# Kernel optimization log

Hardware: AMD Instinct MI355X
Metric: run time of the kernel (lower is better)

## Reference

```python
import jax, jax.numpy as jnp
import numpy as np

B, C, R, E = 8192, 32, 24, 128
NUM_LOC = 100000
NUM_INNER = 200000   # inner_node_embed has NUM_INNER+1 rows; row 0 is padding_idx
NUM_SLICES = 24


def setup_inputs() -> dict:
    key = jax.random.key(0)
    ks = jax.random.split(key, 7)
    context = jax.random.randint(ks[0], (B, C), 0, NUM_LOC)
    route = jax.random.randint(ks[1], (B, R), 0, NUM_INNER + 1)
    lr = jax.random.randint(ks[2], (B, R), 0, 2)
    slice_idx = jax.random.randint(ks[3], (B,), 0, NUM_SLICES)
    input_embed = jax.random.normal(ks[4], (NUM_LOC, E), dtype=jnp.float32)
    inner_node_embed = jax.random.normal(ks[5], (NUM_INNER + 1, E), dtype=jnp.float32).at[0].set(0.0)
    slice_node_embed = jax.random.uniform(ks[6], (NUM_SLICES, E), dtype=jnp.float32)
    return {
        "context": context, "route": route, "lr": lr, "slice_idx": slice_idx,
        "input_embed": input_embed, "inner_node_embed": inner_node_embed,
        "slice_node_embed": slice_node_embed,
    }


def reference(context, route, lr, slice_idx, input_embed, inner_node_embed, slice_node_embed):
    # context embedding: gather + sum over context window -> (B, E)
    ctx = input_embed[context].sum(axis=1)
    # slice prediction: (B, num_slices) softmax, gather target slice prob -> (B,)
    slice_logits = jnp.einsum('se,be->bs', slice_node_embed, ctx)
    slice_prob = jax.nn.softmax(slice_logits, axis=1)
    slice_pre = jnp.take_along_axis(slice_prob, slice_idx[:, None], axis=1)[:, 0]
    # route scores: (B, R)
    dot = jnp.einsum('bre,be->br', inner_node_embed[route], ctx)
    lr_pre = jax.nn.sigmoid(dot)
    # (2p)^lr - p  -> p if lr==1, (1-p) if lr==0
    route_hidden = jnp.power(2.0 * lr_pre, lr.astype(lr_pre.dtype)) - lr_pre
    # padded route positions (route id == 0) contribute factor 1
    route_hidden = jnp.where(route == 0, jnp.ones((), lr_pre.dtype), route_hidden)
    # per-level product loop collapsed into a single prod over route dim
    pr_route = slice_pre * jnp.prod(route_hidden, axis=1)
    return 1.0 - pr_route.mean()
```

## Files before the change

### kernel.cpp

```cpp
#include <hip/hip_runtime.h>

#define BATCH    8192
#define CTX      32
#define ROUTES   24
#define EDIM     128
#define NSLICE   24
#define WPB      4
#define NBLOCKS  (BATCH / WPB)

__device__ __forceinline__ float packed_sum24(const float (&p)[24], const int lane)
{
    float c[12];
    #pragma unroll
    for (int i = 0; i < 12; ++i) {
        const float e0 = p[2*i]   + __shfl_xor(p[2*i],   32);
        const float e1 = p[2*i+1] + __shfl_xor(p[2*i+1], 32);
        c[i] = (lane & 32) ? e1 : e0;
    }
    float d[6];
    #pragma unroll
    for (int i = 0; i < 6; ++i) {
        const float e0 = c[2*i]   + __shfl_xor(c[2*i],   16);
        const float e1 = c[2*i+1] + __shfl_xor(c[2*i+1], 16);
        d[i] = (lane & 16) ? e1 : e0;
    }
    float e[3];
    #pragma unroll
    for (int i = 0; i < 3; ++i) {
        const float e0 = d[2*i]   + __shfl_xor(d[2*i],   8);
        const float e1 = d[2*i+1] + __shfl_xor(d[2*i+1], 8);
        e[i] = (lane & 8) ? e1 : e0;
    }
    const float f0a = e[0] + __shfl_xor(e[0], 4);
    const float f0b = e[1] + __shfl_xor(e[1], 4);
    const float f0  = (lane & 4) ? f0b : f0a;
    const float f1  = (lane & 4) ? 0.f : (e[2] + __shfl_xor(e[2], 4));
    const float g0 = f0 + __shfl_xor(f0, 2);
    const float g1 = f1 + __shfl_xor(f1, 2);
    float g = (lane & 2) ? g1 : g0;
    g += __shfl_xor(g, 1);
    return g;
}

__global__ __launch_bounds__(256, 4) void tale_fused(
    const int* __restrict__ context,
    const int* __restrict__ route,
    const int* __restrict__ lr,
    const int* __restrict__ slice_idx,
    const float* __restrict__ input_embed,
    const float* __restrict__ inner_node_embed,
    const float* __restrict__ slice_node_embed,
    float* __restrict__ out)
{
    const int tid  = threadIdx.x;
    const int lane = tid & 63;
    const int w    = tid >> 6;
    const int b    = __builtin_amdgcn_readfirstlane(blockIdx.x * WPB + w);

    __shared__ float bs[WPB];

    const int voff = lane << 1;

    const int v = ((lane >> 5) & 1) | (((lane >> 4) & 1) << 1) |
                  (((lane >> 3) & 1) << 2) | (((lane >> 2) & 1) << 3) |
                  (((lane >> 1) & 1) << 4);
    const bool vvalid = (v < ROUTES);
    const int  vcl    = vvalid ? v : 0;

    const int rv = route[b * ROUTES + vcl];
    const int lv = lr[b * ROUTES + vcl];
    const int si = slice_idx[b];

    float a0x=0.f,a0y=0.f,a1x=0.f,a1y=0.f,a2x=0.f,a2y=0.f,a3x=0.f,a3y=0.f;
    #pragma unroll
    for (int i = 0; i < CTX; i += 4) {
        const int i0 = context[b * CTX + i + 0];
        const int i1 = context[b * CTX + i + 1];
        const int i2 = context[b * CTX + i + 2];
        const int i3 = context[b * CTX + i + 3];
        const float2 r0 = *reinterpret_cast<const float2*>(input_embed + (size_t)i0 * EDIM + voff);
        const float2 r1 = *reinterpret_cast<const float2*>(input_embed + (size_t)i1 * EDIM + voff);
        const float2 r2 = *reinterpret_cast<const float2*>(input_embed + (size_t)i2 * EDIM + voff);
        const float2 r3 = *reinterpret_cast<const float2*>(input_embed + (size_t)i3 * EDIM + voff);
        a0x += r0.x; a0y += r0.y;
        a1x += r1.x; a1y += r1.y;
        a2x += r2.x; a2y += r2.y;
        a3x += r3.x; a3y += r3.y;
    }
    const float ax = (a0x + a1x) + (a2x + a3x);
    const float ay = (a0y + a1y) + (a2y + a3y);

    float p[24];
    #pragma unroll
    for (int r = 0; r < ROUTES; ++r) {
        const int idx = route[b * ROUTES + r];
        const float2 t = *reinterpret_cast<const float2*>(
            inner_node_embed + (size_t)idx * EDIM + voff);
        p[r] = t.x * ax + t.y * ay;
    }
    const float dotv = packed_sum24(p, lane);

    float q[24];
    #pragma unroll
    for (int s = 0; s < NSLICE; ++s) {
        const float2 t = *reinterpret_cast<const float2*>(
            slice_node_embed + s * EDIM + voff);
        q[s] = t.x * ax + t.y * ay;
    }
    const float logv = packed_sum24(q, lane);

    const float sg = 1.f / (1.f + __expf(-dotv));
    float h = lv ? sg : (1.f - sg);
    if (!vvalid || rv == 0 || (lane & 1)) h = 1.f;
    h *= __shfl_xor(h, 32);
    h *= __shfl_xor(h, 16);
    h *= __shfl_xor(h, 8);
    h *= __shfl_xor(h, 4);
    h *= __shfl_xor(h, 2);
    h *= __shfl_xor(h, 1);
    const float prodv = h;

    float ml = vvalid ? logv : -3.0e38f;
    ml = fmaxf(ml, __shfl_xor(ml, 32));
    ml = fmaxf(ml, __shfl_xor(ml, 16));
    ml = fmaxf(ml, __shfl_xor(ml, 8));
    ml = fmaxf(ml, __shfl_xor(ml, 4));
    ml = fmaxf(ml, __shfl_xor(ml, 2));
    ml = fmaxf(ml, __shfl_xor(ml, 1));
    float ev = (vvalid && !(lane & 1)) ? __expf(logv - ml) : 0.f;
    float den = ev;
    den += __shfl_xor(den, 32);
    den += __shfl_xor(den, 16);
    den += __shfl_xor(den, 8);
    den += __shfl_xor(den, 4);
    den += __shfl_xor(den, 2);
    den += __shfl_xor(den, 1);
    const int lsel = (((si >> 4) & 1) << 1) | (((si >> 3) & 1) << 2) |
                     (((si >> 2) & 1) << 3) | (((si >> 1) & 1) << 4) |
                     ((si & 1) << 5);
    const float esel = __shfl(ev, lsel);
    const float pr = (esel / den) * prodv;

    if (lane == 0) bs[w] = pr;
    __syncthreads();
    if (tid == 0) {
        const float s = (bs[0] + bs[1]) + (bs[2] + bs[3]);
        atomicAdd(out, 1.0f / NBLOCKS - s * (1.0f / BATCH));
    }
}

extern "C" void kernel_launch(void* const* d_in, const int* in_sizes, int n_in,
                              void* d_out, int out_size, void* d_ws, size_t ws_size,
                              hipStream_t stream)
{
    const int*   context          = (const int*)  d_in[0];
    const int*   route            = (const int*)  d_in[1];
    const int*   lr               = (const int*)  d_in[2];
    const int*   slice_idx        = (const int*)  d_in[3];
    const float* input_embed      = (const float*)d_in[4];
    const float* inner_node_embed = (const float*)d_in[5];
    const float* slice_node_embed = (const float*)d_in[6];
    float* out = (float*)d_out;

    hipMemsetAsync(out, 0, sizeof(float), stream);

    tale_fused<<<NBLOCKS, 64 * WPB, 0, stream>>>(
        context, route, lr, slice_idx,
        input_embed, inner_node_embed, slice_node_embed, out);
}
```

Before: 202.8 us.

## Split wavefront into half-waves with float4 row loads and halved shuffle reductions

Each wavefront now works as two 32-lane halves. Each lane loads a float4 slice of an embedding row, and the two halves handle alternating context, route and slice rows, which replaces the float2 loads where every lane touched every row. This halves the per-lane gather instruction count and roughly halves the shuffle-based packed reduction (12 values per lane instead of 24). It adds a cross-half reduction of the context sum, and launch bounds are raised to 8 blocks per CU to increase occupancy, which could pressure registers.

```diff
diff --git a/kernel.cpp b/kernel.cpp
--- a/kernel.cpp
+++ b/kernel.cpp
@@ -8,41 +8,39 @@
 #define WPB      4
 #define NBLOCKS  (BATCH / WPB)
 
-__device__ __forceinline__ float packed_sum24(const float (&p)[24], const int lane)
+__device__ __forceinline__ float dot4(const float4 a, const float4 b)
 {
-    float c[12];
-    #pragma unroll
-    for (int i = 0; i < 12; ++i) {
-        const float e0 = p[2*i]   + __shfl_xor(p[2*i],   32);
-        const float e1 = p[2*i+1] + __shfl_xor(p[2*i+1], 32);
-        c[i] = (lane & 32) ? e1 : e0;
-    }
-    float d[6];
+    return a.x * b.x + a.y * b.y + a.z * b.z + a.w * b.w;
+}
+
+__device__ __forceinline__ float packed_sum12(const float (&p)[12], const int sub)
+{
+    float c[6];
     #pragma unroll
     for (int i = 0; i < 6; ++i) {
-        const float e0 = c[2*i]   + __shfl_xor(c[2*i],   16);
-        const float e1 = c[2*i+1] + __shfl_xor(c[2*i+1], 16);
-        d[i] = (lane & 16) ? e1 : e0;
+        const float e0 = p[2*i]   + __shfl_xor(p[2*i],   16);
+        const float e1 = p[2*i+1] + __shfl_xor(p[2*i+1], 16);
+        c[i] = (sub & 16) ? e1 : e0;
     }
-    float e[3];
+    float d[3];
     #pragma unroll
     for (int i = 0; i < 3; ++i) {
-        const float e0 = d[2*i]   + __shfl_xor(d[2*i],   8);
-        const float e1 = d[2*i+1] + __shfl_xor(d[2*i+1], 8);
-        e[i] = (lane & 8) ? e1 : e0;
+        const float e0 = c[2*i]   + __shfl_xor(c[2*i],   8);
+        const float e1 = c[2*i+1] + __shfl_xor(c[2*i+1], 8);
+        d[i] = (sub & 8) ? e1 : e0;
     }
-    const float f0a = e[0] + __shfl_xor(e[0], 4);
-    const float f0b = e[1] + __shfl_xor(e[1], 4);
-    const float f0  = (lane & 4) ? f0b : f0a;
-    const float f1  = (lane & 4) ? 0.f : (e[2] + __shfl_xor(e[2], 4));
-    const float g0 = f0 + __shfl_xor(f0, 2);
-    const float g1 = f1 + __shfl_xor(f1, 2);
-    float g = (lane & 2) ? g1 : g0;
+    const float e0a = d[0] + __shfl_xor(d[0], 4);
+    const float e0b = d[1] + __shfl_xor(d[1], 4);
+    const float e0  = (sub & 4) ? e0b : e0a;
+    const float e1  = (sub & 4) ? 0.f : (d[2] + __shfl_xor(d[2], 4));
+    const float f0  = e0 + __shfl_xor(e0, 2);
+    const float f1  = e1 + __shfl_xor(e1, 2);
+    float g = (sub & 2) ? f1 : f0;
     g += __shfl_xor(g, 1);
     return g;
 }
 
-__global__ __launch_bounds__(256, 4) void tale_fused(
+__global__ __launch_bounds__(256, 8) void tale_fused(
     const int* __restrict__ context,
     const int* __restrict__ route,
     const int* __restrict__ lr,
@@ -54,90 +52,97 @@
 {
     const int tid  = threadIdx.x;
     const int lane = tid & 63;
+    const int half = lane >> 5;
+    const int sub  = lane & 31;
     const int w    = tid >> 6;
     const int b    = __builtin_amdgcn_readfirstlane(blockIdx.x * WPB + w);
 
     __shared__ float bs[WPB];
 
-    const int voff = lane << 1;
+    const int v = ((sub >> 4) & 1) | (((sub >> 3) & 1) << 1) |
+                  (((sub >> 2) & 1) << 2) | (((sub >> 1) & 1) << 3);
+    const bool vvalid = (v < 12);
+    const int  d      = 2 * v + half;
+    const int  dcl    = vvalid ? d : 0;
 
-    const int v = ((lane >> 5) & 1) | (((lane >> 4) & 1) << 1) |
-                  (((lane >> 3) & 1) << 2) | (((lane >> 2) & 1) << 3) |
-                  (((lane >> 1) & 1) << 4);
-    const bool vvalid = (v < ROUTES);
-    const int  vcl    = vvalid ? v : 0;
+    const int rv  = route[b * ROUTES + dcl];
+    const int lvv = lr[b * ROUTES + dcl];
+    const int si  = slice_idx[b];
 
-    const int rv = route[b * ROUTES + vcl];
-    const int lv = lr[b * ROUTES + vcl];
-    const int si = slice_idx[b];
+    float4 acc0 = make_float4(0.f, 0.f, 0.f, 0.f);
+    float4 acc1 = make_float4(0.f, 0.f, 0.f, 0.f);
+    #pragma unroll
+    for (int i = 0; i < 16; i += 2) {
+        const int a_lo = context[b * CTX + 2*i + 0];
+        const int a_hi = context[b * CTX + 2*i + 1];
+        const int b_lo = context[b * CTX + 2*i + 2];
+        const int b_hi = context[b * CTX + 2*i + 3];
+        const int ia = half ? a_hi : a_lo;
+        const int ib = half ? b_hi : b_lo;
+        const float4 ra = *reinterpret_cast<const float4*>(
+            input_embed + (size_t)ia * EDIM + (sub << 2));
+        const float4 rb = *reinterpret_cast<const float4*>(
+            input_embed + (size_t)ib * EDIM + (sub << 2));
+        acc0.x += ra.x; acc0.y += ra.y; acc0.z += ra.z; acc0.w += ra.w;
+        acc1.x += rb.x; acc1.y += rb.y; acc1.z += rb.z; acc1.w += rb.w;
+    }
+    float4 acc = make_float4(acc0.x + acc1.x, acc0.y + acc1.y,
+                             acc0.z + acc1.z, acc0.w + acc1.w);
+    acc.x += __shfl_xor(acc.x, 32);
+    acc.y += __shfl_xor(acc.y, 32);
+    acc.z += __shfl_xor(acc.z, 32);
+    acc.w += __shfl_xor(acc.w, 32);
 
-    float a0x=0.f,a0y=0.f,a1x=0.f,a1y=0.f,a2x=0.f,a2y=0.f,a3x=0.f,a3y=0.f;
+    float p[12];
     #pragma unroll
-    for (int i = 0; i < CTX; i += 4) {
-        const int i0 = context[b * CTX + i + 0];
-        const int i1 = context[b * CTX + i + 1];
-        const int i2 = context[b * CTX + i + 2];
-        const int i3 = context[b * CTX + i + 3];
-        const float2 r0 = *reinterpret_cast<const float2*>(input_embed + (size_t)i0 * EDIM + voff);
-        const float2 r1 = *reinterpret_cast<const float2*>(input_embed + (size_t)i1 * EDIM + voff);
-        const float2 r2 = *reinterpret_cast<const float2*>(input_embed + (size_t)i2 * EDIM + voff);
-        const float2 r3 = *reinterpret_cast<const float2*>(input_embed + (size_t)i3 * EDIM + voff);
-        a0x += r0.x; a0y += r0.y;
-        a1x += r1.x; a1y += r1.y;
-        a2x += r2.x; a2y += r2.y;
-        a3x += r3.x; a3y += r3.y;
+    for (int i = 0; i < 12; ++i) {
+        const int i_lo = route[b * ROUTES + 2*i + 0];
+        const int i_hi = route[b * ROUTES + 2*i + 1];
+        const int idx  = half ? i_hi : i_lo;
+        const float4 t = *reinterpret_cast<const float4*>(
+            inner_node_embed + (size_t)idx * EDIM + (sub << 2));
+        p[i] = dot4(t, acc);
     }
-    const float ax = (a0x + a1x) + (a2x + a3x);
-    const float ay = (a0y + a1y) + (a2y + a3y);
-
-    float p[24];
-    #pragma unroll
-    for (int r = 0; r < ROUTES; ++r) {
-        const int idx = route[b * ROUTES + r];
-        const float2 t = *reinterpret_cast<const float2*>(
-            inner_node_embed + (size_t)idx * EDIM + voff);
-        p[r] = t.x * ax + t.y * ay;
-    }
-    const float dotv = packed_sum24(p, lane);
-
-    float q[24];
-    #pragma unroll
-    for (int s = 0; s < NSLICE; ++s) {
-        const float2 t = *reinterpret_cast<const float2*>(
-            slice_node_embed + s * EDIM + voff);
-        q[s] = t.x * ax + t.y * ay;
-    }
-    const float logv = packed_sum24(q, lane);
+    const float dotv = packed_sum12(p, sub);
 
     const float sg = 1.f / (1.f + __expf(-dotv));
-    float h = lv ? sg : (1.f - sg);
-    if (!vvalid || rv == 0 || (lane & 1)) h = 1.f;
-    h *= __shfl_xor(h, 32);
+    float h = lvv ? sg : (1.f - sg);
+    if (!vvalid || rv == 0 || (sub & 1)) h = 1.f;
     h *= __shfl_xor(h, 16);
     h *= __shfl_xor(h, 8);
     h *= __shfl_xor(h, 4);
     h *= __shfl_xor(h, 2);
     h *= __shfl_xor(h, 1);
+    h *= __shfl_xor(h, 32);
     const float prodv = h;
 
+    float q[12];
+    #pragma unroll
+    for (int i = 0; i < 12; ++i) {
+        const float4 t = *reinterpret_cast<const float4*>(
+            slice_node_embed + (2*i + half) * EDIM + (sub << 2));
+        q[i] = dot4(t, acc);
+    }
+    const float logv = packed_sum12(q, sub);
+
     float ml = vvalid ? logv : -3.0e38f;
-    ml = fmaxf(ml, __shfl_xor(ml, 32));
     ml = fmaxf(ml, __shfl_xor(ml, 16));
     ml = fmaxf(ml, __shfl_xor(ml, 8));
     ml = fmaxf(ml, __shfl_xor(ml, 4));
     ml = fmaxf(ml, __shfl_xor(ml, 2));
     ml = fmaxf(ml, __shfl_xor(ml, 1));
-    float ev = (vvalid && !(lane & 1)) ? __expf(logv - ml) : 0.f;
+    ml = fmaxf(ml, __shfl_xor(ml, 32));
+    const float ev = (vvalid && !(sub & 1)) ? __expf(logv - ml) : 0.f;
     float den = ev;
-    den += __shfl_xor(den, 32);
     den += __shfl_xor(den, 16);
     den += __shfl_xor(den, 8);
     den += __shfl_xor(den, 4);
     den += __shfl_xor(den, 2);
     den += __shfl_xor(den, 1);
-    const int lsel = (((si >> 4) & 1) << 1) | (((si >> 3) & 1) << 2) |
-                     (((si >> 2) & 1) << 3) | (((si >> 1) & 1) << 4) |
-                     ((si & 1) << 5);
+    den += __shfl_xor(den, 32);
+    const int vt   = si >> 1;
+    const int lsel = ((si & 1) << 5) | ((vt & 1) << 4) | (((vt >> 1) & 1) << 3) |
+                     (((vt >> 2) & 1) << 2) | (((vt >> 3) & 1) << 1);
     const float esel = __shfl(ev, lsel);
     const float pr = (esel / den) * prodv;
 
```

New measurement: 201.0 us. About the same (-0.9%).
